# Optimization experiments

Hardware: AMD Instinct MI355X
Metric: run time of the kernel (lower is better)

The kernel has to match this reference:

```python
import jax, jax.numpy as jnp
import numpy as np

N_NODES = 100000
N_EDGES = 1600000
IN_F = 256
OUT_F = 128


def setup_inputs() -> dict:
    key = jax.random.key(0)
    k1, k2, k3, k4, k5, k6 = jax.random.split(key, 6)
    x = jax.random.normal(k1, (N_NODES, IN_F), dtype=jnp.float32)
    edge_src = jax.random.randint(k2, (N_EDGES,), 0, N_NODES, dtype=jnp.int64)
    edge_dst = jax.random.randint(k3, (N_EDGES,), 0, N_NODES, dtype=jnp.int64)
    edge_weight = jax.random.uniform(k4, (N_EDGES,), dtype=jnp.float32)
    stdv = 1.0 / np.sqrt(OUT_F)
    w = jax.random.uniform(k5, (IN_F, OUT_F), dtype=jnp.float32, minval=-stdv, maxval=stdv)
    b = jax.random.uniform(k6, (OUT_F,), dtype=jnp.float32, minval=-stdv, maxval=stdv)
    return {"x": x, "edge_src": edge_src, "edge_dst": edge_dst,
            "edge_weight": edge_weight, "w": w, "b": b}


def reference(x, edge_src, edge_dst, edge_weight, w, b):
    # dense feature transform: [N, in] @ [in, out] -> [N, out]
    h = x @ w
    # sparse adjacency SpMM: out[i] = sum_{e: dst[e]==i} a[e] * h[src[e]]
    msgs = h[edge_src] * edge_weight[:, None]          # [E, out]
    agg = jax.ops.segment_sum(msgs, edge_dst, num_segments=N_NODES)
    return agg + b
```

## Files before the change

kernel.cpp:

```cpp
#include <hip/hip_runtime.h>

#define N_NODES 100000
#define N_EDGES 1600000
#define IN_F 256
#define OUT_F 128

#define NBUCK 1563
#define NCH   250
#define CH    6400
#define BCAP  2048

typedef __attribute__((ext_vector_type(8))) short bf16x8;
typedef __attribute__((ext_vector_type(4))) float f32x4;

static __device__ __forceinline__ unsigned f2bf_u(float f) {
    unsigned u = __float_as_uint(f);
    return (u + 0x7FFFu + ((u >> 16) & 1u)) >> 16;
}
static __device__ __forceinline__ float bf2f(short s) {
    return __uint_as_float(((unsigned)(unsigned short)s) << 16);
}

__global__ __launch_bounds__(1024) void init_kernel(int* __restrict__ gadd,
                                                    const float* __restrict__ w,
                                                    unsigned short* __restrict__ wtf) {
    const int t = threadIdx.x;
    if (blockIdx.x == 0) {
        for (int i = t; i < NBUCK; i += 1024) gadd[i] = 0;
        return;
    }
    const int id = (blockIdx.x - 1) * 1024 + t;
    const int f = id >> 6, lane = id & 63;
    const int ks = f >> 3, nt = f & 7;
    const int m = lane & 15, q = lane >> 4;
    const int row = nt * 16 + m;
    const int col0 = ks * 32 + q * 8;
    unsigned short* o = wtf + (size_t)f * 512 + lane * 8;
    #pragma unroll
    for (int j = 0; j < 8; ++j)
        o[j] = (unsigned short)f2bf_u(w[(size_t)(col0 + j) * OUT_F + row]);
}

__global__ __launch_bounds__(1024) void part_kernel(const int* __restrict__ edge_src,
                                                    const int* __restrict__ edge_dst,
                                                    const float* __restrict__ edge_weight,
                                                    int* __restrict__ gadd,
                                                    int2* __restrict__ part) {
    __shared__ int h[NBUCK];
    const int t = threadIdx.x;
    const int c = blockIdx.x;
    for (int i = t; i < NBUCK; i += 1024) h[i] = 0;
    __syncthreads();

    const int e0 = c * CH;
    const int4*   d4 = (const int4*)(edge_dst + e0);
    const int4*   s4 = (const int4*)(edge_src + e0);
    const float4* w4 = (const float4*)(edge_weight + e0);

    for (int k = t; k < CH / 4; k += 1024) {
        const int4 dd = d4[k];
        atomicAdd(&h[dd.x >> 6], 1);
        atomicAdd(&h[dd.y >> 6], 1);
        atomicAdd(&h[dd.z >> 6], 1);
        atomicAdd(&h[dd.w >> 6], 1);
    }
    __syncthreads();

    for (int i = t; i < NBUCK; i += 1024) {
        const int cnt = h[i];
        int base = 0;
        if (cnt > 0) base = atomicAdd(&gadd[i], cnt);
        h[i] = i * BCAP + base;
    }
    __syncthreads();

    for (int k = t; k < CH / 4; k += 1024) {
        const int4   dd = d4[k];
        const int4   ss = s4[k];
        const float4 ww = w4[k];
        int b, pos;
        b = dd.x >> 6; pos = atomicAdd(&h[b], 1);
        if (pos < (b + 1) * BCAP)
            part[pos] = make_int2(ss.x | ((dd.x & 63) << 24), __float_as_int(ww.x));
        b = dd.y >> 6; pos = atomicAdd(&h[b], 1);
        if (pos < (b + 1) * BCAP)
            part[pos] = make_int2(ss.y | ((dd.y & 63) << 24), __float_as_int(ww.y));
        b = dd.z >> 6; pos = atomicAdd(&h[b], 1);
        if (pos < (b + 1) * BCAP)
            part[pos] = make_int2(ss.z | ((dd.z & 63) << 24), __float_as_int(ww.z));
        b = dd.w >> 6; pos = atomicAdd(&h[b], 1);
        if (pos < (b + 1) * BCAP)
            part[pos] = make_int2(ss.w | ((dd.w & 63) << 24), __float_as_int(ww.w));
    }
}

__global__ __launch_bounds__(256) void gemm_mfma_kernel(const float* __restrict__ x,
                                                        const unsigned short* __restrict__ wtf,
                                                        unsigned short* __restrict__ hb) {
    __shared__ unsigned short xs[64][264];
    const int t = threadIdx.x;
    const int row0 = blockIdx.x * 64;

    const float4* x4 = (const float4*)x;
    #pragma unroll
    for (int i = 0; i < 16; ++i) {
        int idx = t + i * 256;
        int r = idx >> 6, c4 = idx & 63;
        int rg = row0 + r; if (rg >= N_NODES) rg = N_NODES - 1;
        float4 v = x4[(size_t)rg * 64 + c4];
        unsigned u0 = f2bf_u(v.x) | (f2bf_u(v.y) << 16);
        unsigned u1 = f2bf_u(v.z) | (f2bf_u(v.w) << 16);
        *(uint2*)&xs[r][c4 * 4] = make_uint2(u0, u1);
    }
    __syncthreads();

    const int wave = t >> 6, lane = t & 63;
    const int m = lane & 15, quad = lane >> 4;

    bf16x8 af[8];
    #pragma unroll
    for (int ks = 0; ks < 8; ++ks)
        af[ks] = *(const bf16x8*)&xs[wave * 16 + m][ks * 32 + quad * 8];

    f32x4 acc[8];
    #pragma unroll
    for (int nt = 0; nt < 8; ++nt) acc[nt] = (f32x4){0.f, 0.f, 0.f, 0.f};

    const bf16x8* wf = (const bf16x8*)wtf;
    #pragma unroll
    for (int ks = 0; ks < 8; ++ks) {
        #pragma unroll
        for (int nt = 0; nt < 8; ++nt) {
            bf16x8 bf = wf[(size_t)(ks * 8 + nt) * 64 + lane];
            acc[nt] = __builtin_amdgcn_mfma_f32_16x16x32_bf16(af[ks], bf, acc[nt], 0, 0, 0);
        }
    }

    const int tile_base = row0 + wave * 16;
    #pragma unroll
    for (int nt = 0; nt < 8; ++nt) {
        #pragma unroll
        for (int r = 0; r < 4; ++r) {
            int orow = tile_base + quad * 4 + r;
            if (orow < N_NODES)
                hb[(size_t)orow * OUT_F + nt * 16 + m] = (unsigned short)f2bf_u(acc[nt][r]);
        }
    }
}

__global__ __launch_bounds__(512) void spmm_kernel(const unsigned short* __restrict__ hb,
                                                   const int* __restrict__ gadd,
                                                   const int2* __restrict__ part,
                                                   const float* __restrict__ b,
                                                   float* __restrict__ out) {
    __shared__ int lh[64];
    __shared__ int lstart[65];
    __shared__ int lcur[64];
    __shared__ int2 list[BCAP];

    const int t = threadIdx.x;
    const int bucket = blockIdx.x;
    const int base = bucket * 64;

    int cntb = gadd[bucket];
    if (cntb > BCAP) cntb = BCAP;
    const size_t s0 = (size_t)bucket * BCAP;

    if (t < 64) lh[t] = 0;
    __syncthreads();

    int2 stash[4];
    int  sn[4];
    #pragma unroll
    for (int sub = 0; sub < 4; ++sub) {
        const int idx = sub * 512 + t;
        sn[sub] = -1;
        if (idx < cntb) {
            const int2 en = part[s0 + idx];
            const int n = ((unsigned)en.x) >> 24;
            sn[sub] = n;
            stash[sub] = make_int2(en.x & 0xFFFFFF, en.y);
            atomicAdd(&lh[n], 1);
        }
    }
    __syncthreads();

    if (t < 64) {
        const int v = lh[t];
        int s = v;
        #pragma unroll
        for (int off = 1; off < 64; off <<= 1) {
            const int o = __shfl_up(s, off);
            if (t >= off) s += o;
        }
        lstart[t] = s - v;
        lcur[t]   = s - v;
        if (t == 63) lstart[64] = s;
    }
    __syncthreads();

    #pragma unroll
    for (int sub = 0; sub < 4; ++sub) {
        if (sn[sub] >= 0) {
            const int pos = atomicAdd(&lcur[sn[sub]], 1);
            list[pos] = stash[sub];
        }
    }
    __syncthreads();

    const int j = t & 15;
    const float4* b4 = (const float4*)b;
    const float4 bb0 = b4[j * 2];
    const float4 bb1 = b4[j * 2 + 1];

    #pragma unroll
    for (int g = 0; g < 2; ++g) {
        const int n = g * 32 + (t >> 4);
        const int node = base + n;
        if (node >= N_NODES) continue;
        float4 acc0 = bb0, acc1 = bb1;
        int p = lstart[n];
        const int p1 = lstart[n + 1];
        for (; p + 4 <= p1; p += 4) {
            const int2 sw0 = list[p];
            const int2 sw1 = list[p + 1];
            const int2 sw2 = list[p + 2];
            const int2 sw3 = list[p + 3];
            const bf16x8 h0 = *(const bf16x8*)(hb + (size_t)sw0.x * OUT_F + j * 8);
            const bf16x8 h1 = *(const bf16x8*)(hb + (size_t)sw1.x * OUT_F + j * 8);
            const bf16x8 h2 = *(const bf16x8*)(hb + (size_t)sw2.x * OUT_F + j * 8);
            const bf16x8 h3 = *(const bf16x8*)(hb + (size_t)sw3.x * OUT_F + j * 8);
            const float w0 = __int_as_float(sw0.y);
            const float w1 = __int_as_float(sw1.y);
            const float w2 = __int_as_float(sw2.y);
            const float w3 = __int_as_float(sw3.y);
            acc0.x += w0 * bf2f(h0[0]); acc0.y += w0 * bf2f(h0[1]);
            acc0.z += w0 * bf2f(h0[2]); acc0.w += w0 * bf2f(h0[3]);
            acc1.x += w0 * bf2f(h0[4]); acc1.y += w0 * bf2f(h0[5]);
            acc1.z += w0 * bf2f(h0[6]); acc1.w += w0 * bf2f(h0[7]);
            acc0.x += w1 * bf2f(h1[0]); acc0.y += w1 * bf2f(h1[1]);
            acc0.z += w1 * bf2f(h1[2]); acc0.w += w1 * bf2f(h1[3]);
            acc1.x += w1 * bf2f(h1[4]); acc1.y += w1 * bf2f(h1[5]);
            acc1.z += w1 * bf2f(h1[6]); acc1.w += w1 * bf2f(h1[7]);
            acc0.x += w2 * bf2f(h2[0]); acc0.y += w2 * bf2f(h2[1]);
            acc0.z += w2 * bf2f(h2[2]); acc0.w += w2 * bf2f(h2[3]);
            acc1.x += w2 * bf2f(h2[4]); acc1.y += w2 * bf2f(h2[5]);
            acc1.z += w2 * bf2f(h2[6]); acc1.w += w2 * bf2f(h2[7]);
            acc0.x += w3 * bf2f(h3[0]); acc0.y += w3 * bf2f(h3[1]);
            acc0.z += w3 * bf2f(h3[2]); acc0.w += w3 * bf2f(h3[3]);
            acc1.x += w3 * bf2f(h3[4]); acc1.y += w3 * bf2f(h3[5]);
            acc1.z += w3 * bf2f(h3[6]); acc1.w += w3 * bf2f(h3[7]);
        }
        for (; p < p1; ++p) {
            const int2 sw = list[p];
            const float wgt = __int_as_float(sw.y);
            const bf16x8 hv = *(const bf16x8*)(hb + (size_t)sw.x * OUT_F + j * 8);
            acc0.x += wgt * bf2f(hv[0]); acc0.y += wgt * bf2f(hv[1]);
            acc0.z += wgt * bf2f(hv[2]); acc0.w += wgt * bf2f(hv[3]);
            acc1.x += wgt * bf2f(hv[4]); acc1.y += wgt * bf2f(hv[5]);
            acc1.z += wgt * bf2f(hv[6]); acc1.w += wgt * bf2f(hv[7]);
        }
        float4* o4 = (float4*)(out + (size_t)node * OUT_F + j * 8);
        o4[0] = acc0;
        o4[1] = acc1;
    }
}

extern "C" void kernel_launch(void* const* d_in, const int* in_sizes, int n_in,
                              void* d_out, int out_size, void* d_ws, size_t ws_size,
                              hipStream_t stream) {
    const float* x           = (const float*)d_in[0];
    const int*   edge_src    = (const int*)d_in[1];
    const int*   edge_dst    = (const int*)d_in[2];
    const float* edge_weight = (const float*)d_in[3];
    const float* w           = (const float*)d_in[4];
    const float* b           = (const float*)d_in[5];
    float* out = (float*)d_out;

    char* ws = (char*)d_ws;
    size_t off = 0;
    unsigned short* hb  = (unsigned short*)(ws + off);
    off += (size_t)N_NODES * OUT_F * 2;           off = (off + 15) & ~(size_t)15;
    unsigned short* wtf = (unsigned short*)(ws + off);
    off += (size_t)IN_F * OUT_F * 2;              off = (off + 15) & ~(size_t)15;
    int* gadd = (int*)(ws + off);
    off += (size_t)NBUCK * 4;                     off = (off + 15) & ~(size_t)15;
    int2* part = (int2*)(ws + off);
    off += (size_t)NBUCK * BCAP * 8;

    init_kernel<<<5, 1024, 0, stream>>>(gadd, w, wtf);
    part_kernel<<<NCH, 1024, 0, stream>>>(edge_src, edge_dst, edge_weight, gadd, part);
    gemm_mfma_kernel<<<(N_NODES + 63) / 64, 256, 0, stream>>>(x, wtf, hb);
    spmm_kernel<<<NBUCK, 512, 0, stream>>>(hb, gadd, part, b, out);
}
```

Measured before the change: 289.1 us.

## Fuse edge partitioning and GEMM into one interleaved launch

Combines the edge bucketing kernel and the bf16 MFMA GEMM into one launch. Every fourth block does partitioning and the rest do GEMM tiles, with the GEMM tile grown to 128 rows and 512 threads. Shared memory is a union of the histogram and the x tile. The aim is to overlap the latency-bound, atomic-heavy partition step with the compute and bandwidth-bound GEMM and to remove one launch. In exchange, the partition blocks now have half the threads and the larger shared footprint may lower occupancy.

```diff
diff --git a/kernel.cpp b/kernel.cpp
--- a/kernel.cpp
+++ b/kernel.cpp
@@ -9,6 +9,8 @@
 #define NCH   250
 #define CH    6400
 #define BCAP  2048
+#define NTILE 782
+#define NFUSE 1044
 
 typedef __attribute__((ext_vector_type(8))) short bf16x8;
 typedef __attribute__((ext_vector_type(4))) float f32x4;
@@ -41,76 +43,86 @@
         o[j] = (unsigned short)f2bf_u(w[(size_t)(col0 + j) * OUT_F + row]);
 }
 
-__global__ __launch_bounds__(1024) void part_kernel(const int* __restrict__ edge_src,
+union SMem {
+    int h[NBUCK];
+    unsigned short xs[128][264];
+};
+
+__global__ __launch_bounds__(512) void fused_kernel(const int* __restrict__ edge_src,
                                                     const int* __restrict__ edge_dst,
                                                     const float* __restrict__ edge_weight,
                                                     int* __restrict__ gadd,
-                                                    int2* __restrict__ part) {
-    __shared__ int h[NBUCK];
+                                                    int2* __restrict__ part,
+                                                    const float* __restrict__ x,
+                                                    const unsigned short* __restrict__ wtf,
+                                                    unsigned short* __restrict__ hb) {
+    __shared__ SMem sm;
     const int t = threadIdx.x;
-    const int c = blockIdx.x;
-    for (int i = t; i < NBUCK; i += 1024) h[i] = 0;
-    __syncthreads();
-
-    const int e0 = c * CH;
-    const int4*   d4 = (const int4*)(edge_dst + e0);
-    const int4*   s4 = (const int4*)(edge_src + e0);
-    const float4* w4 = (const float4*)(edge_weight + e0);
-
-    for (int k = t; k < CH / 4; k += 1024) {
-        const int4 dd = d4[k];
-        atomicAdd(&h[dd.x >> 6], 1);
-        atomicAdd(&h[dd.y >> 6], 1);
-        atomicAdd(&h[dd.z >> 6], 1);
-        atomicAdd(&h[dd.w >> 6], 1);
-    }
-    __syncthreads();
-
-    for (int i = t; i < NBUCK; i += 1024) {
-        const int cnt = h[i];
-        int base = 0;
-        if (cnt > 0) base = atomicAdd(&gadd[i], cnt);
-        h[i] = i * BCAP + base;
-    }
-    __syncthreads();
-
-    for (int k = t; k < CH / 4; k += 1024) {
-        const int4   dd = d4[k];
-        const int4   ss = s4[k];
-        const float4 ww = w4[k];
-        int b, pos;
-        b = dd.x >> 6; pos = atomicAdd(&h[b], 1);
-        if (pos < (b + 1) * BCAP)
-            part[pos] = make_int2(ss.x | ((dd.x & 63) << 24), __float_as_int(ww.x));
-        b = dd.y >> 6; pos = atomicAdd(&h[b], 1);
-        if (pos < (b + 1) * BCAP)
-            part[pos] = make_int2(ss.y | ((dd.y & 63) << 24), __float_as_int(ww.y));
-        b = dd.z >> 6; pos = atomicAdd(&h[b], 1);
-        if (pos < (b + 1) * BCAP)
-            part[pos] = make_int2(ss.z | ((dd.z & 63) << 24), __float_as_int(ww.z));
-        b = dd.w >> 6; pos = atomicAdd(&h[b], 1);
-        if (pos < (b + 1) * BCAP)
-            part[pos] = make_int2(ss.w | ((dd.w & 63) << 24), __float_as_int(ww.w));
-    }
-}
-
-__global__ __launch_bounds__(256) void gemm_mfma_kernel(const float* __restrict__ x,
-                                                        const unsigned short* __restrict__ wtf,
-                                                        unsigned short* __restrict__ hb) {
-    __shared__ unsigned short xs[64][264];
-    const int t = threadIdx.x;
-    const int row0 = blockIdx.x * 64;
+    const int bid = blockIdx.x;
+
+    if ((bid & 3) == 0) {
+        const int c = bid >> 2;
+        if (c >= NCH) return;
+        for (int i = t; i < NBUCK; i += 512) sm.h[i] = 0;
+        __syncthreads();
+
+        const int e0 = c * CH;
+        const int4*   d4 = (const int4*)(edge_dst + e0);
+        const int4*   s4 = (const int4*)(edge_src + e0);
+        const float4* w4 = (const float4*)(edge_weight + e0);
+
+        for (int k = t; k < CH / 4; k += 512) {
+            const int4 dd = d4[k];
+            atomicAdd(&sm.h[dd.x >> 6], 1);
+            atomicAdd(&sm.h[dd.y >> 6], 1);
+            atomicAdd(&sm.h[dd.z >> 6], 1);
+            atomicAdd(&sm.h[dd.w >> 6], 1);
+        }
+        __syncthreads();
+
+        for (int i = t; i < NBUCK; i += 512) {
+            const int cnt = sm.h[i];
+            int base = 0;
+            if (cnt > 0) base = atomicAdd(&gadd[i], cnt);
+            sm.h[i] = i * BCAP + base;
+        }
+        __syncthreads();
+
+        for (int k = t; k < CH / 4; k += 512) {
+            const int4   dd = d4[k];
+            const int4   ss = s4[k];
+            const float4 ww = w4[k];
+            int b, pos;
+            b = dd.x >> 6; pos = atomicAdd(&sm.h[b], 1);
+            if (pos < (b + 1) * BCAP)
+                part[pos] = make_int2(ss.x | ((dd.x & 63) << 24), __float_as_int(ww.x));
+            b = dd.y >> 6; pos = atomicAdd(&sm.h[b], 1);
+            if (pos < (b + 1) * BCAP)
+                part[pos] = make_int2(ss.y | ((dd.y & 63) << 24), __float_as_int(ww.y));
+            b = dd.z >> 6; pos = atomicAdd(&sm.h[b], 1);
+            if (pos < (b + 1) * BCAP)
+                part[pos] = make_int2(ss.z | ((dd.z & 63) << 24), __float_as_int(ww.z));
+            b = dd.w >> 6; pos = atomicAdd(&sm.h[b], 1);
+            if (pos < (b + 1) * BCAP)
+                part[pos] = make_int2(ss.w | ((dd.w & 63) << 24), __float_as_int(ww.w));
+        }
+        return;
+    }
+
+    const int tile = bid - (bid >> 2) - 1;
+    if (tile >= NTILE) return;
+    const int row0 = tile * 128;
 
     const float4* x4 = (const float4*)x;
     #pragma unroll
     for (int i = 0; i < 16; ++i) {
-        int idx = t + i * 256;
+        int idx = t + i * 512;
         int r = idx >> 6, c4 = idx & 63;
         int rg = row0 + r; if (rg >= N_NODES) rg = N_NODES - 1;
         float4 v = x4[(size_t)rg * 64 + c4];
         unsigned u0 = f2bf_u(v.x) | (f2bf_u(v.y) << 16);
         unsigned u1 = f2bf_u(v.z) | (f2bf_u(v.w) << 16);
-        *(uint2*)&xs[r][c4 * 4] = make_uint2(u0, u1);
+        *(uint2*)&sm.xs[r][c4 * 4] = make_uint2(u0, u1);
     }
     __syncthreads();
 
@@ -120,7 +132,7 @@
     bf16x8 af[8];
     #pragma unroll
     for (int ks = 0; ks < 8; ++ks)
-        af[ks] = *(const bf16x8*)&xs[wave * 16 + m][ks * 32 + quad * 8];
+        af[ks] = *(const bf16x8*)&sm.xs[wave * 16 + m][ks * 32 + quad * 8];
 
     f32x4 acc[8];
     #pragma unroll
@@ -289,7 +301,7 @@
     off += (size_t)NBUCK * BCAP * 8;
 
     init_kernel<<<5, 1024, 0, stream>>>(gadd, w, wtf);
-    part_kernel<<<NCH, 1024, 0, stream>>>(edge_src, edge_dst, edge_weight, gadd, part);
-    gemm_mfma_kernel<<<(N_NODES + 63) / 64, 256, 0, stream>>>(x, wtf, hb);
+    fused_kernel<<<NFUSE, 512, 0, stream>>>(edge_src, edge_dst, edge_weight, gadd, part,
+                                            x, wtf, hb);
     spmm_kernel<<<NBUCK, 512, 0, stream>>>(hb, gadd, part, b, out);
 }
```

Result: no change. 293.2 us (+1.4%).

## Load GEMM A-fragments directly from global, 32 rows per wave; cache edges in part_kernel

Applied to the files above, without the earlier changes.

The GEMM kernel no longer stages x through LDS. Each wave now loads its bf16 A fragments straight from global memory and computes two 16-row tiles, so each W fragment load is reused across two MFMAs and the block covers 128 rows. The partition kernel keeps the edge dst/src/weight loads in registers from the histogram pass and reuses them in the scatter pass instead of reading them from global twice. The direct global loads give less coalesced x access per lane (32-byte strided chunks), and register pressure goes up.

```diff
diff --git a/kernel.cpp b/kernel.cpp
--- a/kernel.cpp
+++ b/kernel.cpp
@@ -19,6 +19,14 @@
 }
 static __device__ __forceinline__ float bf2f(short s) {
     return __uint_as_float(((unsigned)(unsigned short)s) << 16);
+}
+static __device__ __forceinline__ bf16x8 pack_bf16x8(float4 a, float4 b) {
+    union { unsigned u[4]; bf16x8 v; } r;
+    r.u[0] = f2bf_u(a.x) | (f2bf_u(a.y) << 16);
+    r.u[1] = f2bf_u(a.z) | (f2bf_u(a.w) << 16);
+    r.u[2] = f2bf_u(b.x) | (f2bf_u(b.y) << 16);
+    r.u[3] = f2bf_u(b.z) | (f2bf_u(b.w) << 16);
+    return r.v;
 }
 
 __global__ __launch_bounds__(1024) void init_kernel(int* __restrict__ gadd,
@@ -57,12 +65,23 @@
     const int4*   s4 = (const int4*)(edge_src + e0);
     const float4* w4 = (const float4*)(edge_weight + e0);
 
-    for (int k = t; k < CH / 4; k += 1024) {
-        const int4 dd = d4[k];
-        atomicAdd(&h[dd.x >> 6], 1);
-        atomicAdd(&h[dd.y >> 6], 1);
-        atomicAdd(&h[dd.z >> 6], 1);
-        atomicAdd(&h[dd.w >> 6], 1);
+    int4   dd[2];
+    int4   ss[2];
+    float4 ww[2];
+    bool   val[2];
+    #pragma unroll
+    for (int i = 0; i < 2; ++i) {
+        const int k = t + i * 1024;
+        val[i] = (k < CH / 4);
+        if (val[i]) {
+            dd[i] = d4[k];
+            ss[i] = s4[k];
+            ww[i] = w4[k];
+            atomicAdd(&h[dd[i].x >> 6], 1);
+            atomicAdd(&h[dd[i].y >> 6], 1);
+            atomicAdd(&h[dd[i].z >> 6], 1);
+            atomicAdd(&h[dd[i].w >> 6], 1);
+        }
     }
     __syncthreads();
 
@@ -74,76 +93,69 @@
     }
     __syncthreads();
 
-    for (int k = t; k < CH / 4; k += 1024) {
-        const int4   dd = d4[k];
-        const int4   ss = s4[k];
-        const float4 ww = w4[k];
-        int b, pos;
-        b = dd.x >> 6; pos = atomicAdd(&h[b], 1);
-        if (pos < (b + 1) * BCAP)
-            part[pos] = make_int2(ss.x | ((dd.x & 63) << 24), __float_as_int(ww.x));
-        b = dd.y >> 6; pos = atomicAdd(&h[b], 1);
-        if (pos < (b + 1) * BCAP)
-            part[pos] = make_int2(ss.y | ((dd.y & 63) << 24), __float_as_int(ww.y));
-        b = dd.z >> 6; pos = atomicAdd(&h[b], 1);
-        if (pos < (b + 1) * BCAP)
-            part[pos] = make_int2(ss.z | ((dd.z & 63) << 24), __float_as_int(ww.z));
-        b = dd.w >> 6; pos = atomicAdd(&h[b], 1);
-        if (pos < (b + 1) * BCAP)
-            part[pos] = make_int2(ss.w | ((dd.w & 63) << 24), __float_as_int(ww.w));
+    #pragma unroll
+    for (int i = 0; i < 2; ++i) {
+        if (val[i]) {
+            int b, pos;
+            b = dd[i].x >> 6; pos = atomicAdd(&h[b], 1);
+            if (pos < (b + 1) * BCAP)
+                part[pos] = make_int2(ss[i].x | ((dd[i].x & 63) << 24), __float_as_int(ww[i].x));
+            b = dd[i].y >> 6; pos = atomicAdd(&h[b], 1);
+            if (pos < (b + 1) * BCAP)
+                part[pos] = make_int2(ss[i].y | ((dd[i].y & 63) << 24), __float_as_int(ww[i].y));
+            b = dd[i].z >> 6; pos = atomicAdd(&h[b], 1);
+            if (pos < (b + 1) * BCAP)
+                part[pos] = make_int2(ss[i].z | ((dd[i].z & 63) << 24), __float_as_int(ww[i].z));
+            b = dd[i].w >> 6; pos = atomicAdd(&h[b], 1);
+            if (pos < (b + 1) * BCAP)
+                part[pos] = make_int2(ss[i].w | ((dd[i].w & 63) << 24), __float_as_int(ww[i].w));
+        }
     }
 }
 
 __global__ __launch_bounds__(256) void gemm_mfma_kernel(const float* __restrict__ x,
                                                         const unsigned short* __restrict__ wtf,
                                                         unsigned short* __restrict__ hb) {
-    __shared__ unsigned short xs[64][264];
     const int t = threadIdx.x;
-    const int row0 = blockIdx.x * 64;
-
-    const float4* x4 = (const float4*)x;
-    #pragma unroll
-    for (int i = 0; i < 16; ++i) {
-        int idx = t + i * 256;
-        int r = idx >> 6, c4 = idx & 63;
-        int rg = row0 + r; if (rg >= N_NODES) rg = N_NODES - 1;
-        float4 v = x4[(size_t)rg * 64 + c4];
-        unsigned u0 = f2bf_u(v.x) | (f2bf_u(v.y) << 16);
-        unsigned u1 = f2bf_u(v.z) | (f2bf_u(v.w) << 16);
-        *(uint2*)&xs[r][c4 * 4] = make_uint2(u0, u1);
-    }
-    __syncthreads();
-
     const int wave = t >> 6, lane = t & 63;
     const int m = lane & 15, quad = lane >> 4;
-
-    bf16x8 af[8];
-    #pragma unroll
-    for (int ks = 0; ks < 8; ++ks)
-        af[ks] = *(const bf16x8*)&xs[wave * 16 + m][ks * 32 + quad * 8];
-
-    f32x4 acc[8];
-    #pragma unroll
-    for (int nt = 0; nt < 8; ++nt) acc[nt] = (f32x4){0.f, 0.f, 0.f, 0.f};
+    const int row0 = blockIdx.x * 128 + wave * 32;
+
+    int rA = row0 + m;      if (rA >= N_NODES) rA = N_NODES - 1;
+    int rB = row0 + 16 + m; if (rB >= N_NODES) rB = N_NODES - 1;
+    const float4* xA = (const float4*)(x + (size_t)rA * IN_F) + quad * 2;
+    const float4* xB = (const float4*)(x + (size_t)rB * IN_F) + quad * 2;
+
+    f32x4 acc[2][8];
+    #pragma unroll
+    for (int tl = 0; tl < 2; ++tl)
+        #pragma unroll
+        for (int nt = 0; nt < 8; ++nt) acc[tl][nt] = (f32x4){0.f, 0.f, 0.f, 0.f};
 
     const bf16x8* wf = (const bf16x8*)wtf;
     #pragma unroll
     for (int ks = 0; ks < 8; ++ks) {
+        const bf16x8 a0 = pack_bf16x8(xA[ks * 8], xA[ks * 8 + 1]);
+        const bf16x8 a1 = pack_bf16x8(xB[ks * 8], xB[ks * 8 + 1]);
         #pragma unroll
         for (int nt = 0; nt < 8; ++nt) {
-            bf16x8 bf = wf[(size_t)(ks * 8 + nt) * 64 + lane];
-            acc[nt] = __builtin_amdgcn_mfma_f32_16x16x32_bf16(af[ks], bf, acc[nt], 0, 0, 0);
-        }
-    }
-
-    const int tile_base = row0 + wave * 16;
-    #pragma unroll
-    for (int nt = 0; nt < 8; ++nt) {
+            const bf16x8 bf = wf[(size_t)(ks * 8 + nt) * 64 + lane];
+            acc[0][nt] = __builtin_amdgcn_mfma_f32_16x16x32_bf16(a0, bf, acc[0][nt], 0, 0, 0);
+            acc[1][nt] = __builtin_amdgcn_mfma_f32_16x16x32_bf16(a1, bf, acc[1][nt], 0, 0, 0);
+        }
+    }
+
+    #pragma unroll
+    for (int tl = 0; tl < 2; ++tl) {
+        const int tile_base = row0 + tl * 16;
         #pragma unroll
-        for (int r = 0; r < 4; ++r) {
-            int orow = tile_base + quad * 4 + r;
-            if (orow < N_NODES)
-                hb[(size_t)orow * OUT_F + nt * 16 + m] = (unsigned short)f2bf_u(acc[nt][r]);
+        for (int nt = 0; nt < 8; ++nt) {
+            #pragma unroll
+            for (int r = 0; r < 4; ++r) {
+                const int orow = tile_base + quad * 4 + r;
+                if (orow < N_NODES)
+                    hb[(size_t)orow * OUT_F + nt * 16 + m] = (unsigned short)f2bf_u(acc[tl][nt][r]);
+            }
         }
     }
 }
@@ -290,6 +302,6 @@
 
     init_kernel<<<5, 1024, 0, stream>>>(gadd, w, wtf);
     part_kernel<<<NCH, 1024, 0, stream>>>(edge_src, edge_dst, edge_weight, gadd, part);
-    gemm_mfma_kernel<<<(N_NODES + 63) / 64, 256, 0, stream>>>(x, wtf, hb);
+    gemm_mfma_kernel<<<(N_NODES + 127) / 128, 256, 0, stream>>>(x, wtf, hb);
     spmm_kernel<<<NBUCK, 512, 0, stream>>>(hb, gadd, part, b, out);
 }
```

After: 285.4 us. No clear change (-1.3%).
